# Optimization experiments

Measured on AMD Instinct MI355X. Metric: run time of the kernel, lower is better.

## Reference

```python
import jax, jax.numpy as jnp
import numpy as np

B, L, D, N = 4, 8192, 128, 32


def setup_inputs() -> dict:
    key = jax.random.key(0)
    ks = jax.random.split(key, 12)
    s = 0.05  # small init scale for stability of exp/cumsum
    return {
        "x": jax.random.normal(ks[0], (B, L, D), jnp.float32),
        "h_t_minus_1": jax.random.normal(ks[1], (B, L, D), jnp.float32),
        "A_log": jax.random.normal(ks[2], (D, N), jnp.float32),
        "D_param": jnp.ones((D,), jnp.float32),
        "W_x": jax.random.normal(ks[3], (D, 2 * N + D), jnp.float32) * s,
        "W_dt": jax.random.normal(ks[4], (D, D), jnp.float32) * s,
        "b_dt": jnp.zeros((D,), jnp.float32),
        "conv_w": jax.random.normal(ks[5], (3, D, D), jnp.float32) * s,  # (width, in, out)
        "conv_b": jnp.zeros((D,), jnp.float32),
        "W_f": jax.random.normal(ks[6], (D, D), jnp.float32) * s,
        "b_f": jnp.zeros((D,), jnp.float32),
    }


def reference(x, h_t_minus_1, A_log, D_param, W_x, W_dt, b_dt, conv_w, conv_b, W_f, b_f):
    d, n = A_log.shape
    A = -jnp.exp(A_log)  # (d, n)
    x_dbl = x @ W_x  # (b, l, d + 2n)
    delta, Bm, Cm = jnp.split(x_dbl, [d, d + n], axis=-1)
    delta = jax.nn.softplus(delta @ W_dt + b_dt)  # (b, l, d)

    # selective scan
    dA = jnp.einsum('bld,dn->bldn', delta, A)
    dB_u = jnp.einsum('bld,bld,bln->bldn', delta, h_t_minus_1, Bm)
    dA_cumsum = jnp.exp(jnp.cumsum(dA, axis=1) - dA)  # exclusive cumsum
    h_t = jnp.einsum('bldn,bln->bld', dB_u * dA_cumsum, Cm)
    h_t = h_t + h_t * D_param

    ssm_output = jax.nn.relu(h_t @ W_f + b_f)
    # causal Conv1D, kernel=3: left-pad by 2
    conv = jax.lax.conv_general_dilated(
        ssm_output, conv_w, window_strides=(1,), padding=[(2, 0)],
        dimension_numbers=('NWC', 'WIO', 'NWC')) + conv_b
    causal_output = jax.nn.relu(conv)
    fused_output = ssm_output * causal_output
    return (fused_output, h_t)
```

## Files before the change

kernel.cpp:

```cpp
#include <hip/hip_runtime.h>
#include <math.h>

typedef unsigned short u16;
typedef __attribute__((ext_vector_type(8))) short short8v;
typedef __attribute__((ext_vector_type(4))) float f32x4;

constexpr int B_  = 4;
constexpr int L_  = 8192;
constexpr int D_  = 128;
constexpr int N_  = 32;
constexpr int BL  = B_ * L_;
constexpr int CH  = 16;
constexpr int NC  = L_ / CH;
constexpr int SCH = 32;
constexpr int SNC = L_ / SCH;

__device__ inline unsigned bfr(float x) {
    unsigned u = __float_as_uint(x);
    return (u + 0x7fffu + ((u >> 16) & 1u)) >> 16;
}
__device__ inline unsigned pkbf(float a, float b) { return bfr(a) | (bfr(b) << 16); }
__device__ inline float b2f(u16 h) { return __uint_as_float(((unsigned)h) << 16); }

__global__ __launch_bounds__(256) void prep(
    const float* __restrict__ Wx, const float* __restrict__ Wdt,
    const float* __restrict__ Wf, const float* __restrict__ Wconv,
    const float* __restrict__ A_log,
    u16* __restrict__ Wt0, u16* __restrict__ Wt2, u16* __restrict__ Wtc,
    float* __restrict__ negA)
{
    const int which = blockIdx.y;
    const int t = blockIdx.x * 256 + threadIdx.x;
    if (which == 0) {
        if (t >= 128 * 128) return;
        const int d = t >> 7, k = t & 127;
        float s = 0.f;
        for (int j = 0; j < 128; ++j)
            s = fmaf(Wx[(size_t)k * 192 + j], Wdt[(size_t)j * 128 + d], s);
        Wt0[d * 128 + k] = (u16)bfr(s);
    } else if (which == 1) {
        if (t >= 64 * 128) return;
        const int n = t >> 7, k = t & 127;
        Wt0[(128 + n) * 128 + k] = (u16)bfr(Wx[(size_t)k * 192 + 128 + n]);
    } else if (which == 2) {
        if (t >= 128 * 128) return;
        const int n = t >> 7, k = t & 127;
        Wt2[n * 128 + k] = (u16)bfr(Wf[(size_t)k * 128 + n]);
    } else if (which <= 5) {
        if (t >= 128 * 128) return;
        const int w = which - 3;
        const int n = t >> 7, k = t & 127;
        Wtc[((size_t)w * 128 + n) * 128 + k] = (u16)bfr(Wconv[((size_t)w * 128 + k) * 128 + n]);
    } else {
        if (t < D_ * N_) negA[t] = -expf(A_log[t]) * 1.4426950408889634f;
    }
}

__global__ __launch_bounds__(512) void gemm1(
    const float* __restrict__ x, const u16* __restrict__ Wt0,
    const float* __restrict__ b_dt,
    float* __restrict__ delta, float* __restrict__ bc, float* __restrict__ part)
{
    __shared__ __align__(16) u16 Alds[64 * 64];
    __shared__ __align__(16) u16 Blds[192 * 64];

    const int tid = threadIdx.x;
    const int r0 = blockIdx.x * 64;
    const int wid = tid >> 6, lane = tid & 63;
    const int wm = wid >> 1, wn = wid & 1;
    const int lr = lane & 15, kg = lane >> 4;

    f32x4 acc[6] = {};

    for (int kt = 0; kt < 128; kt += 64) {
        {
            const int row = tid >> 3, k8 = (tid & 7) * 8;
            const float* src = &x[(size_t)(r0 + row) * 128 + kt + k8];
            const float4 v0 = *reinterpret_cast<const float4*>(src);
            const float4 v1 = *reinterpret_cast<const float4*>(src + 4);
            uint4 p;
            p.x = pkbf(v0.x, v0.y); p.y = pkbf(v0.z, v0.w);
            p.z = pkbf(v1.x, v1.y); p.w = pkbf(v1.z, v1.w);
            *reinterpret_cast<uint4*>(&Alds[row * 64 + (k8 ^ ((row & 7) << 3))]) = p;
        }
        #pragma unroll
        for (int j = 0; j < 3; ++j) {
            const int g = tid + j * 512;
            const int n = g >> 3, k8 = (g & 7) * 8;
            const uint4 p = *reinterpret_cast<const uint4*>(&Wt0[(size_t)n * 128 + kt + k8]);
            *reinterpret_cast<uint4*>(&Blds[n * 64 + (k8 ^ ((n & 7) << 3))]) = p;
        }
        __syncthreads();
        #pragma unroll
        for (int ks = 0; ks < 2; ++ks) {
            const int k8 = ks * 32 + kg * 8;
            const int row = wm * 16 + lr;
            const short8v af = *reinterpret_cast<const short8v*>(
                &Alds[row * 64 + (k8 ^ ((row & 7) << 3))]);
            #pragma unroll
            for (int nf = 0; nf < 6; ++nf) {
                const int col = wn * 96 + nf * 16 + lr;
                const short8v bf = *reinterpret_cast<const short8v*>(
                    &Blds[col * 64 + (k8 ^ ((col & 7) << 3))]);
                acc[nf] = __builtin_amdgcn_mfma_f32_16x16x32_bf16(af, bf, acc[nf], 0, 0, 0);
            }
        }
        __syncthreads();
    }

    const int nDelta = wn ? 2 : 6;
    float colsum[6];
    #pragma unroll
    for (int nf = 0; nf < 6; ++nf) {
        if (nf < nDelta) {
            const int col = wn * 96 + nf * 16 + lr;
            const float bb = b_dt[col];
            float s4 = 0.f;
            #pragma unroll
            for (int q = 0; q < 4; ++q) {
                float v = acc[nf][q] + bb;
                v = fmaxf(v, 0.f) + log1pf(expf(-fabsf(v)));
                const int row = r0 + wm * 16 + kg * 4 + q;
                delta[(size_t)row * 128 + col] = v;
                s4 += v;
            }
            colsum[nf] = s4;
        }
    }
    if (wn) {
        #pragma unroll
        for (int h = 0; h < 2; ++h)
            #pragma unroll
            for (int q = 0; q < 4; ++q) {
                const int row = r0 + wm * 16 + kg * 4 + q;
                bc[(size_t)row * 32 + h * 16 + lr] = acc[2 + h][q] * acc[4 + h][q];
            }
    }
    const int b = r0 / L_;
    const int c = (r0 % L_) / CH + wm;
    #pragma unroll
    for (int nf = 0; nf < 6; ++nf) {
        if (nf < nDelta) {
            float s = colsum[nf];
            s += __shfl_xor(s, 16, 64);
            s += __shfl_xor(s, 32, 64);
            if (kg == 0) {
                const int col = wn * 96 + nf * 16 + lr;
                part[((size_t)b * NC + c) * 128 + col] = s;
            }
        }
    }
}

__global__ __launch_bounds__(512) void scan_prefix(float* __restrict__ part)
{
    const int b = blockIdx.x, d = blockIdx.y;
    const int c = threadIdx.x, w = c >> 6, lane = c & 63;
    const size_t idx = ((size_t)b * NC + c) * 128 + d;
    const float v = part[idx];
    float s = v;
    #pragma unroll
    for (int off = 1; off < 64; off <<= 1) {
        const float t = __shfl_up(s, off, 64);
        if (lane >= off) s += t;
    }
    __shared__ float wsum[8];
    if (lane == 63) wsum[w] = s;
    __syncthreads();
    float add = 0.f;
    #pragma unroll
    for (int i = 0; i < 8; ++i)
        if (i < w) add += wsum[i];
    part[idx] = s + add - v;
}

__global__ __launch_bounds__(512) void scan_main(
    const float* __restrict__ delta, const float* __restrict__ hprev,
    const float* __restrict__ bc, const float* __restrict__ negA,
    const float* __restrict__ Dp, const float* __restrict__ part,
    const u16* __restrict__ Wt2, const float* __restrict__ b_f,
    float* __restrict__ h_out, u16* __restrict__ ssm)
{
    __shared__ float delta_s[SCH][128];
    __shared__ float bc_s[SCH][32];
    __shared__ __align__(16) u16 h_s[SCH * 128];

    const int cb = blockIdx.x, b = blockIdx.y;
    const int tid = threadIdx.x;
    const size_t rowbase = (size_t)b * L_ + (size_t)cb * SCH;

    #pragma unroll
    for (int j = 0; j < 2; ++j) {
        const int gg = tid + j * 512;
        const int row = gg >> 5, c4 = (gg & 31) * 4;
        *reinterpret_cast<float4*>(&delta_s[row][c4]) =
            *reinterpret_cast<const float4*>(&delta[(rowbase + row) * 128 + c4]);
    }
    if (tid < 256) {
        const int row = tid >> 3, c4 = (tid & 7) * 4;
        *reinterpret_cast<float4*>(&bc_s[row][c4]) =
            *reinterpret_cast<const float4*>(&bc[(rowbase + row) * 32 + c4]);
    }

    const int d = tid & 127, r0 = tid >> 7;
    float a[N_];
    #pragma unroll
    for (int n4 = 0; n4 < 8; ++n4) {
        const float4 v = *reinterpret_cast<const float4*>(&negA[d * N_ + n4 * 4]);
        a[n4 * 4 + 0] = v.x; a[n4 * 4 + 1] = v.y;
        a[n4 * 4 + 2] = v.z; a[n4 * 4 + 3] = v.w;
    }
    const float dp1 = 1.f + Dp[d];
    float hv[8];
    #pragma unroll
    for (int r = 0; r < 8; ++r)
        hv[r] = hprev[(rowbase + r * 4 + r0) * 128 + d];
    const float sbase = part[((size_t)b * NC + cb * 2) * 128 + d];
    __syncthreads();

    float sv[8];
    {
        float s = sbase;
        #pragma unroll
        for (int i = 0; i < 32; ++i) {
            if ((i & 3) == r0) sv[i >> 2] = s;
            s += delta_s[i][d];
        }
    }
    #pragma unroll
    for (int r = 0; r < 8; ++r) {
        const int i = r * 4 + r0;
        const float dv = delta_s[i][d];
        const float sr = sv[r];
        float p0 = 0.f, p1 = 0.f, p2 = 0.f, p3 = 0.f;
        #pragma unroll
        for (int n = 0; n < N_; n += 4) {
            const float4 b4 = *reinterpret_cast<const float4*>(&bc_s[i][n]);
            p0 = fmaf(b4.x, exp2f(sr * a[n + 0]), p0);
            p1 = fmaf(b4.y, exp2f(sr * a[n + 1]), p1);
            p2 = fmaf(b4.z, exp2f(sr * a[n + 2]), p2);
            p3 = fmaf(b4.w, exp2f(sr * a[n + 3]), p3);
        }
        const float h = dv * hv[r] * ((p0 + p1) + (p2 + p3)) * dp1;
        h_out[(rowbase + i) * 128 + d] = h;
        h_s[i * 128 + (((d >> 3) ^ (i & 7)) << 3) + (d & 7)] = (u16)bfr(h);
    }
    __syncthreads();

    const int wid = tid >> 6, lane = tid & 63;
    const int lr = lane & 15, kg = lane >> 4;
    const int col = wid * 16 + lr;
    f32x4 acc[2] = {};
    #pragma unroll
    for (int ks = 0; ks < 4; ++ks) {
        const int k8 = ks * 32 + kg * 8;
        const short8v bfg = *reinterpret_cast<const short8v*>(&Wt2[(size_t)col * 128 + k8]);
        #pragma unroll
        for (int m = 0; m < 2; ++m) {
            const int row = m * 16 + lr;
            const short8v afg = *reinterpret_cast<const short8v*>(
                &h_s[row * 128 + (k8 ^ ((row & 7) << 3))]);
            acc[m] = __builtin_amdgcn_mfma_f32_16x16x32_bf16(afg, bfg, acc[m], 0, 0, 0);
        }
    }
    const float bb = b_f[col];
    #pragma unroll
    for (int m = 0; m < 2; ++m)
        #pragma unroll
        for (int q = 0; q < 4; ++q) {
            const int row = m * 16 + kg * 4 + q;
            const float v = fmaxf(acc[m][q] + bb, 0.f);
            ssm[(rowbase + row) * 128 + col] = (u16)bfr(v);
        }
}

__global__ __launch_bounds__(512) void conv_fuse(
    const u16* __restrict__ ssm, const u16* __restrict__ Wtc,
    const float* __restrict__ cbias, float* __restrict__ fused)
{
    __shared__ __align__(16) u16 Alds[130 * 128];

    const int tid = threadIdx.x;
    const int bb = blockIdx.y;
    const int r0 = blockIdx.x * 128;
    const u16* sb = ssm + (size_t)bb * L_ * 128;

    #pragma unroll
    for (int j = 0; j < 5; ++j) {
        const int g = tid + j * 512;
        if (g < 130 * 16) {
            const int i = g >> 4, k8 = (g & 15) * 8;
            const int gr = r0 - 2 + i;
            uint4 p = make_uint4(0, 0, 0, 0);
            if (gr >= 0)
                p = *reinterpret_cast<const uint4*>(&sb[(size_t)gr * 128 + k8]);
            *reinterpret_cast<uint4*>(&Alds[i * 128 + (k8 ^ ((i & 7) << 3))]) = p;
        }
    }
    __syncthreads();

    const int wid = tid >> 6, lane = tid & 63;
    const int wm = wid >> 1, wn = wid & 1;
    const int lr = lane & 15, kg = lane >> 4;

    f32x4 acc[2][4] = {};
    #pragma unroll
    for (int ks = 0; ks < 4; ++ks) {
        const int k8 = ks * 32 + kg * 8;
        short8v af[2][3];
        #pragma unroll
        for (int m = 0; m < 2; ++m)
            #pragma unroll
            for (int w = 0; w < 3; ++w) {
                const int ri = wm * 32 + m * 16 + lr + w;
                af[m][w] = *reinterpret_cast<const short8v*>(
                    &Alds[ri * 128 + (k8 ^ ((ri & 7) << 3))]);
            }
        #pragma unroll
        for (int nf = 0; nf < 4; ++nf) {
            const int col = wn * 64 + nf * 16 + lr;
            #pragma unroll
            for (int w = 0; w < 3; ++w) {
                const short8v bfg = *reinterpret_cast<const short8v*>(
                    &Wtc[((size_t)w * 128 + col) * 128 + k8]);
                acc[0][nf] = __builtin_amdgcn_mfma_f32_16x16x32_bf16(af[0][w], bfg, acc[0][nf], 0, 0, 0);
                acc[1][nf] = __builtin_amdgcn_mfma_f32_16x16x32_bf16(af[1][w], bfg, acc[1][nf], 0, 0, 0);
            }
        }
    }

    #pragma unroll
    for (int nf = 0; nf < 4; ++nf) {
        const int col = wn * 64 + nf * 16 + lr;
        const float bb2 = cbias[col];
        #pragma unroll
        for (int m = 0; m < 2; ++m)
            #pragma unroll
            for (int q = 0; q < 4; ++q) {
                const int row = wm * 32 + m * 16 + kg * 4 + q;
                const int ri = row + 2;
                const u16 sh = Alds[ri * 128 + ((((col >> 3) ^ (ri & 7)) << 3)) + (col & 7)];
                const float cv = fmaxf(acc[m][nf][q] + bb2, 0.f);
                fused[((size_t)bb * L_ + r0 + row) * 128 + col] = b2f(sh) * cv;
            }
    }
}

extern "C" void kernel_launch(void* const* d_in, const int* in_sizes, int n_in,
                              void* d_out, int out_size, void* d_ws, size_t ws_size,
                              hipStream_t stream)
{
    const float* x      = (const float*)d_in[0];
    const float* hprev  = (const float*)d_in[1];
    const float* A_log  = (const float*)d_in[2];
    const float* Dp     = (const float*)d_in[3];
    const float* W_x    = (const float*)d_in[4];
    const float* W_dt   = (const float*)d_in[5];
    const float* b_dt   = (const float*)d_in[6];
    const float* conv_w = (const float*)d_in[7];
    const float* conv_b = (const float*)d_in[8];
    const float* W_f    = (const float*)d_in[9];
    const float* b_f    = (const float*)d_in[10];

    float* out   = (float*)d_out;
    float* h_out = out + (size_t)BL * D_;

    char* ws = (char*)d_ws;
    float* delta = (float*)ws;                  ws += (size_t)BL * 128 * 4;
    float* bcb   = (float*)ws;                  ws += (size_t)BL * 32 * 4;
    float* part  = (float*)ws;                  ws += (size_t)B_ * NC * 128 * 4;
    float* negA  = (float*)ws;                  ws += (size_t)D_ * N_ * 4;
    u16*   Wt0   = (u16*)ws;                    ws += (size_t)192 * 128 * 2;
    u16*   Wt2   = (u16*)ws;                    ws += (size_t)128 * 128 * 2;
    u16*   Wtc   = (u16*)ws;                    ws += (size_t)3 * 128 * 128 * 2;
    u16*   ssm   = (u16*)ws;

    prep<<<dim3(64, 7), dim3(256), 0, stream>>>(
        W_x, W_dt, W_f, conv_w, A_log, Wt0, Wt2, Wtc, negA);
    gemm1<<<dim3(BL / 64), dim3(512), 0, stream>>>(
        x, Wt0, b_dt, delta, bcb, part);
    scan_prefix<<<dim3(B_, D_), dim3(512), 0, stream>>>(part);
    scan_main<<<dim3(SNC, B_), dim3(512), 0, stream>>>(
        delta, hprev, bcb, negA, Dp, part, Wt2, b_f, h_out, ssm);
    conv_fuse<<<dim3(L_ / 128, B_), dim3(512), 0, stream>>>(
        ssm, Wtc, conv_b, out);
}
```

Baseline: 175.5 us.

## Reorder scan loops to cut registers, halve conv tile, coalesce prep reads

```diff
diff --git a/kernel.cpp b/kernel.cpp
--- a/kernel.cpp
+++ b/kernel.cpp
@@ -33,7 +33,7 @@
     const int t = blockIdx.x * 256 + threadIdx.x;
     if (which == 0) {
         if (t >= 128 * 128) return;
-        const int d = t >> 7, k = t & 127;
+        const int k = t >> 7, d = t & 127;
         float s = 0.f;
         for (int j = 0; j < 128; ++j)
             s = fmaf(Wx[(size_t)k * 192 + j], Wdt[(size_t)j * 128 + d], s);
@@ -203,13 +203,6 @@
     }
 
     const int d = tid & 127, r0 = tid >> 7;
-    float a[N_];
-    #pragma unroll
-    for (int n4 = 0; n4 < 8; ++n4) {
-        const float4 v = *reinterpret_cast<const float4*>(&negA[d * N_ + n4 * 4]);
-        a[n4 * 4 + 0] = v.x; a[n4 * 4 + 1] = v.y;
-        a[n4 * 4 + 2] = v.z; a[n4 * 4 + 3] = v.w;
-    }
     const float dp1 = 1.f + Dp[d];
     float hv[8];
     #pragma unroll
@@ -227,21 +220,30 @@
             s += delta_s[i][d];
         }
     }
+
+    float p[8] = {};
+    #pragma unroll 2
+    for (int n4 = 0; n4 < 8; ++n4) {
+        const float4 a4 = *reinterpret_cast<const float4*>(&negA[d * N_ + n4 * 4]);
+        #pragma unroll
+        for (int r = 0; r < 8; ++r) {
+            const int i = r * 4 + r0;
+            const float4 b4 = *reinterpret_cast<const float4*>(&bc_s[i][n4 * 4]);
+            const float sr = sv[r];
+            const float e0 = exp2f(sr * a4.x);
+            const float e1 = exp2f(sr * a4.y);
+            const float e2 = exp2f(sr * a4.z);
+            const float e3 = exp2f(sr * a4.w);
+            float t0 = fmaf(b4.x, e0, b4.y * e1);
+            float t1 = fmaf(b4.z, e2, b4.w * e3);
+            p[r] += t0 + t1;
+        }
+    }
+
     #pragma unroll
     for (int r = 0; r < 8; ++r) {
         const int i = r * 4 + r0;
-        const float dv = delta_s[i][d];
-        const float sr = sv[r];
-        float p0 = 0.f, p1 = 0.f, p2 = 0.f, p3 = 0.f;
-        #pragma unroll
-        for (int n = 0; n < N_; n += 4) {
-            const float4 b4 = *reinterpret_cast<const float4*>(&bc_s[i][n]);
-            p0 = fmaf(b4.x, exp2f(sr * a[n + 0]), p0);
-            p1 = fmaf(b4.y, exp2f(sr * a[n + 1]), p1);
-            p2 = fmaf(b4.z, exp2f(sr * a[n + 2]), p2);
-            p3 = fmaf(b4.w, exp2f(sr * a[n + 3]), p3);
-        }
-        const float h = dv * hv[r] * ((p0 + p1) + (p2 + p3)) * dp1;
+        const float h = delta_s[i][d] * hv[r] * p[r] * dp1;
         h_out[(rowbase + i) * 128 + d] = h;
         h_s[i * 128 + (((d >> 3) ^ (i & 7)) << 3) + (d & 7)] = (u16)bfr(h);
     }
@@ -278,17 +280,17 @@
     const u16* __restrict__ ssm, const u16* __restrict__ Wtc,
     const float* __restrict__ cbias, float* __restrict__ fused)
 {
-    __shared__ __align__(16) u16 Alds[130 * 128];
+    __shared__ __align__(16) u16 Alds[66 * 128];
 
     const int tid = threadIdx.x;
     const int bb = blockIdx.y;
-    const int r0 = blockIdx.x * 128;
+    const int r0 = blockIdx.x * 64;
     const u16* sb = ssm + (size_t)bb * L_ * 128;
 
     #pragma unroll
-    for (int j = 0; j < 5; ++j) {
+    for (int j = 0; j < 3; ++j) {
         const int g = tid + j * 512;
-        if (g < 130 * 16) {
+        if (g < 66 * 16) {
             const int i = g >> 4, k8 = (g & 15) * 8;
             const int gr = r0 - 2 + i;
             uint4 p = make_uint4(0, 0, 0, 0);
@@ -300,10 +302,10 @@
     __syncthreads();
 
     const int wid = tid >> 6, lane = tid & 63;
-    const int wm = wid >> 1, wn = wid & 1;
+    const int wm = wid >> 2, wn = wid & 3;
     const int lr = lane & 15, kg = lane >> 4;
 
-    f32x4 acc[2][4] = {};
+    f32x4 acc[2][2] = {};
     #pragma unroll
     for (int ks = 0; ks < 4; ++ks) {
         const int k8 = ks * 32 + kg * 8;
@@ -317,8 +319,8 @@
                     &Alds[ri * 128 + (k8 ^ ((ri & 7) << 3))]);
             }
         #pragma unroll
-        for (int nf = 0; nf < 4; ++nf) {
-            const int col = wn * 64 + nf * 16 + lr;
+        for (int nf = 0; nf < 2; ++nf) {
+            const int col = wn * 32 + nf * 16 + lr;
             #pragma unroll
             for (int w = 0; w < 3; ++w) {
                 const short8v bfg = *reinterpret_cast<const short8v*>(
@@ -330,8 +332,8 @@
     }
 
     #pragma unroll
-    for (int nf = 0; nf < 4; ++nf) {
-        const int col = wn * 64 + nf * 16 + lr;
+    for (int nf = 0; nf < 2; ++nf) {
+        const int col = wn * 32 + nf * 16 + lr;
         const float bb2 = cbias[col];
         #pragma unroll
         for (int m = 0; m < 2; ++m)
@@ -382,6 +384,6 @@
     scan_prefix<<<dim3(B_, D_), dim3(512), 0, stream>>>(part);
     scan_main<<<dim3(SNC, B_), dim3(512), 0, stream>>>(
         delta, hprev, bcb, negA, Dp, part, Wt2, b_f, h_out, ssm);
-    conv_fuse<<<dim3(L_ / 128, B_), dim3(512), 0, stream>>>(
+    conv_fuse<<<dim3(L_ / 64, B_), dim3(512), 0, stream>>>(
         ssm, Wtc, conv_b, out);
 }
```

Result: slower. 179.0 us (+2.0%).

## Restructure pipeline: local prefix in gemm1, row-parallel scan, fuse W_f GEMM into conv

Applied to the files above, without the earlier changes.

```diff
diff --git a/kernel.cpp b/kernel.cpp
--- a/kernel.cpp
+++ b/kernel.cpp
@@ -12,8 +12,6 @@
 constexpr int BL  = B_ * L_;
 constexpr int CH  = 16;
 constexpr int NC  = L_ / CH;
-constexpr int SCH = 32;
-constexpr int SNC = L_ / SCH;
 
 __device__ inline unsigned bfr(float x) {
     unsigned u = __float_as_uint(x);
@@ -22,33 +20,47 @@
 __device__ inline unsigned pkbf(float a, float b) { return bfr(a) | (bfr(b) << 16); }
 __device__ inline float b2f(u16 h) { return __uint_as_float(((unsigned)h) << 16); }
 
-__global__ __launch_bounds__(256) void prep(
+__global__ __launch_bounds__(512) void prep_weff(
     const float* __restrict__ Wx, const float* __restrict__ Wdt,
-    const float* __restrict__ Wf, const float* __restrict__ Wconv,
-    const float* __restrict__ A_log,
+    u16* __restrict__ Wt0)
+{
+    __shared__ float wd[128 * 128];
+    const int tid = threadIdx.x;
+    #pragma unroll
+    for (int j = 0; j < 8; ++j) {
+        const int g = tid + j * 512;
+        *reinterpret_cast<float4*>(&wd[g * 4]) =
+            *reinterpret_cast<const float4*>(&Wdt[(size_t)g * 4]);
+    }
+    __syncthreads();
+    const int k = blockIdx.x * 4 + (tid >> 7);
+    const int d = tid & 127;
+    float s = 0.f;
+    #pragma unroll 8
+    for (int j = 0; j < 128; ++j)
+        s = fmaf(Wx[(size_t)k * 192 + j], wd[j * 128 + d], s);
+    Wt0[d * 128 + k] = (u16)bfr(s);
+}
+
+__global__ __launch_bounds__(256) void prep_rest(
+    const float* __restrict__ Wx, const float* __restrict__ Wf,
+    const float* __restrict__ Wconv, const float* __restrict__ A_log,
     u16* __restrict__ Wt0, u16* __restrict__ Wt2, u16* __restrict__ Wtc,
     float* __restrict__ negA)
 {
     const int which = blockIdx.y;
     const int t = blockIdx.x * 256 + threadIdx.x;
     if (which == 0) {
-        if (t >= 128 * 128) return;
-        const int d = t >> 7, k = t & 127;
-        float s = 0.f;
-        for (int j = 0; j < 128; ++j)
-            s = fmaf(Wx[(size_t)k * 192 + j], Wdt[(size_t)j * 128 + d], s);
-        Wt0[d * 128 + k] = (u16)bfr(s);
-    } else if (which == 1) {
         if (t >= 64 * 128) return;
         const int n = t >> 7, k = t & 127;
         Wt0[(128 + n) * 128 + k] = (u16)bfr(Wx[(size_t)k * 192 + 128 + n]);
-    } else if (which == 2) {
+    } else if (which == 1) {
         if (t >= 128 * 128) return;
         const int n = t >> 7, k = t & 127;
         Wt2[n * 128 + k] = (u16)bfr(Wf[(size_t)k * 128 + n]);
-    } else if (which <= 5) {
+    } else if (which <= 4) {
         if (t >= 128 * 128) return;
-        const int w = which - 3;
+        const int w = which - 2;
         const int n = t >> 7, k = t & 127;
         Wtc[((size_t)w * 128 + n) * 128 + k] = (u16)bfr(Wconv[((size_t)w * 128 + k) * 128 + n]);
     } else {
@@ -56,100 +68,96 @@
     }
 }
 
-__global__ __launch_bounds__(512) void gemm1(
+__global__ __launch_bounds__(256) void gemm1(
     const float* __restrict__ x, const u16* __restrict__ Wt0,
     const float* __restrict__ b_dt,
-    float* __restrict__ delta, float* __restrict__ bc, float* __restrict__ part)
-{
-    __shared__ __align__(16) u16 Alds[64 * 64];
-    __shared__ __align__(16) u16 Blds[192 * 64];
+    float* __restrict__ delta, float* __restrict__ Sloc,
+    float* __restrict__ bc, float* __restrict__ part)
+{
+    __shared__ __align__(16) u16 Blds[192 * 128];
 
     const int tid = threadIdx.x;
     const int r0 = blockIdx.x * 64;
-    const int wid = tid >> 6, lane = tid & 63;
-    const int wm = wid >> 1, wn = wid & 1;
+
+    #pragma unroll
+    for (int j = 0; j < 12; ++j) {
+        const int g = tid + j * 256;
+        const int n = g >> 4, k8 = (g & 15) * 8;
+        const uint4 p = *reinterpret_cast<const uint4*>(&Wt0[(size_t)n * 128 + k8]);
+        *reinterpret_cast<uint4*>(&Blds[n * 128 + (k8 ^ ((n & 7) << 3))]) = p;
+    }
+
+    const int w = tid >> 6, lane = tid & 63;
     const int lr = lane & 15, kg = lane >> 4;
-
-    f32x4 acc[6] = {};
-
-    for (int kt = 0; kt < 128; kt += 64) {
-        {
-            const int row = tid >> 3, k8 = (tid & 7) * 8;
-            const float* src = &x[(size_t)(r0 + row) * 128 + kt + k8];
-            const float4 v0 = *reinterpret_cast<const float4*>(src);
-            const float4 v1 = *reinterpret_cast<const float4*>(src + 4);
-            uint4 p;
-            p.x = pkbf(v0.x, v0.y); p.y = pkbf(v0.z, v0.w);
-            p.z = pkbf(v1.x, v1.y); p.w = pkbf(v1.z, v1.w);
-            *reinterpret_cast<uint4*>(&Alds[row * 64 + (k8 ^ ((row & 7) << 3))]) = p;
-        }
-        #pragma unroll
-        for (int j = 0; j < 3; ++j) {
-            const int g = tid + j * 512;
-            const int n = g >> 3, k8 = (g & 7) * 8;
-            const uint4 p = *reinterpret_cast<const uint4*>(&Wt0[(size_t)n * 128 + kt + k8]);
-            *reinterpret_cast<uint4*>(&Blds[n * 64 + (k8 ^ ((n & 7) << 3))]) = p;
-        }
-        __syncthreads();
-        #pragma unroll
-        for (int ks = 0; ks < 2; ++ks) {
-            const int k8 = ks * 32 + kg * 8;
-            const int row = wm * 16 + lr;
-            const short8v af = *reinterpret_cast<const short8v*>(
-                &Alds[row * 64 + (k8 ^ ((row & 7) << 3))]);
-            #pragma unroll
-            for (int nf = 0; nf < 6; ++nf) {
-                const int col = wn * 96 + nf * 16 + lr;
-                const short8v bf = *reinterpret_cast<const short8v*>(
-                    &Blds[col * 64 + (k8 ^ ((col & 7) << 3))]);
-                acc[nf] = __builtin_amdgcn_mfma_f32_16x16x32_bf16(af, bf, acc[nf], 0, 0, 0);
-            }
-        }
-        __syncthreads();
-    }
-
-    const int nDelta = wn ? 2 : 6;
-    float colsum[6];
-    #pragma unroll
-    for (int nf = 0; nf < 6; ++nf) {
-        if (nf < nDelta) {
-            const int col = wn * 96 + nf * 16 + lr;
-            const float bb = b_dt[col];
-            float s4 = 0.f;
-            #pragma unroll
-            for (int q = 0; q < 4; ++q) {
-                float v = acc[nf][q] + bb;
-                v = fmaxf(v, 0.f) + log1pf(expf(-fabsf(v)));
-                const int row = r0 + wm * 16 + kg * 4 + q;
-                delta[(size_t)row * 128 + col] = v;
-                s4 += v;
-            }
-            colsum[nf] = s4;
-        }
-    }
-    if (wn) {
-        #pragma unroll
-        for (int h = 0; h < 2; ++h)
-            #pragma unroll
-            for (int q = 0; q < 4; ++q) {
-                const int row = r0 + wm * 16 + kg * 4 + q;
-                bc[(size_t)row * 32 + h * 16 + lr] = acc[2 + h][q] * acc[4 + h][q];
-            }
-    }
-    const int b = r0 / L_;
-    const int c = (r0 % L_) / CH + wm;
-    #pragma unroll
-    for (int nf = 0; nf < 6; ++nf) {
-        if (nf < nDelta) {
-            float s = colsum[nf];
-            s += __shfl_xor(s, 16, 64);
-            s += __shfl_xor(s, 32, 64);
-            if (kg == 0) {
-                const int col = wn * 96 + nf * 16 + lr;
-                part[((size_t)b * NC + c) * 128 + col] = s;
-            }
-        }
-    }
+    const int arow = r0 + w * 16 + lr;
+
+    float4 av[4][2];
+    #pragma unroll
+    for (int ks = 0; ks < 4; ++ks) {
+        const float* src = &x[(size_t)arow * 128 + ks * 32 + kg * 8];
+        av[ks][0] = *reinterpret_cast<const float4*>(src);
+        av[ks][1] = *reinterpret_cast<const float4*>(src + 4);
+    }
+    __syncthreads();
+
+    f32x4 acc[12] = {};
+    #pragma unroll
+    for (int ks = 0; ks < 4; ++ks) {
+        uint4 ap;
+        ap.x = pkbf(av[ks][0].x, av[ks][0].y);
+        ap.y = pkbf(av[ks][0].z, av[ks][0].w);
+        ap.z = pkbf(av[ks][1].x, av[ks][1].y);
+        ap.w = pkbf(av[ks][1].z, av[ks][1].w);
+        const short8v af = *reinterpret_cast<const short8v*>(&ap);
+        const int kb = ks * 32 + kg * 8;
+        #pragma unroll
+        for (int nf = 0; nf < 12; ++nf) {
+            const int n = nf * 16 + lr;
+            const short8v bf = *reinterpret_cast<const short8v*>(
+                &Blds[n * 128 + (kb ^ ((n & 7) << 3))]);
+            acc[nf] = __builtin_amdgcn_mfma_f32_16x16x32_bf16(af, bf, acc[nf], 0, 0, 0);
+        }
+    }
+
+    const int orow = r0 + w * 16;
+    const size_t chunkb = (size_t)(orow / CH) * 128;
+    #pragma unroll
+    for (int nf = 0; nf < 8; ++nf) {
+        const int col = nf * 16 + lr;
+        const float bb = b_dt[col];
+        float v[4];
+        #pragma unroll
+        for (int q = 0; q < 4; ++q) {
+            const float t = acc[nf][q] + bb;
+            v[q] = fmaxf(t, 0.f) + log1pf(expf(-fabsf(t)));
+        }
+        const float e1 = v[0], e2 = e1 + v[1], e3 = e2 + v[2];
+        const float g4 = e3 + v[3];
+        const float g0 = __shfl(g4, lr, 64);
+        const float g1 = __shfl(g4, lr + 16, 64);
+        const float g2 = __shfl(g4, lr + 32, 64);
+        const float g3 = __shfl(g4, lr + 48, 64);
+        float base = 0.f;
+        if (kg > 0) base += g0;
+        if (kg > 1) base += g1;
+        if (kg > 2) base += g2;
+        const size_t rb = (size_t)(orow + kg * 4) * 128 + col;
+        delta[rb + 0 * 128] = v[0];
+        delta[rb + 1 * 128] = v[1];
+        delta[rb + 2 * 128] = v[2];
+        delta[rb + 3 * 128] = v[3];
+        Sloc[rb + 0 * 128] = base;
+        Sloc[rb + 1 * 128] = base + e1;
+        Sloc[rb + 2 * 128] = base + e2;
+        Sloc[rb + 3 * 128] = base + e3;
+        if (kg == 0) part[chunkb + col] = g0 + g1 + g2 + g3;
+    }
+    #pragma unroll
+    for (int h = 0; h < 2; ++h)
+        #pragma unroll
+        for (int q = 0; q < 4; ++q)
+            bc[(size_t)(orow + kg * 4 + q) * 32 + h * 16 + lr] =
+                acc[8 + h][q] * acc[10 + h][q];
 }
 
 __global__ __launch_bounds__(512) void scan_prefix(float* __restrict__ part)
@@ -174,35 +182,15 @@
     part[idx] = s + add - v;
 }
 
-__global__ __launch_bounds__(512) void scan_main(
-    const float* __restrict__ delta, const float* __restrict__ hprev,
-    const float* __restrict__ bc, const float* __restrict__ negA,
-    const float* __restrict__ Dp, const float* __restrict__ part,
-    const u16* __restrict__ Wt2, const float* __restrict__ b_f,
-    float* __restrict__ h_out, u16* __restrict__ ssm)
-{
-    __shared__ float delta_s[SCH][128];
-    __shared__ float bc_s[SCH][32];
-    __shared__ __align__(16) u16 h_s[SCH * 128];
-
-    const int cb = blockIdx.x, b = blockIdx.y;
+__global__ __launch_bounds__(512) void scan_h(
+    const float* __restrict__ delta, const float* __restrict__ Sloc,
+    const float* __restrict__ hprev, const float* __restrict__ bc,
+    const float* __restrict__ negA, const float* __restrict__ Dp,
+    const float* __restrict__ part,
+    float* __restrict__ h_out, u16* __restrict__ hb)
+{
     const int tid = threadIdx.x;
-    const size_t rowbase = (size_t)b * L_ + (size_t)cb * SCH;
-
-    #pragma unroll
-    for (int j = 0; j < 2; ++j) {
-        const int gg = tid + j * 512;
-        const int row = gg >> 5, c4 = (gg & 31) * 4;
-        *reinterpret_cast<float4*>(&delta_s[row][c4]) =
-            *reinterpret_cast<const float4*>(&delta[(rowbase + row) * 128 + c4]);
-    }
-    if (tid < 256) {
-        const int row = tid >> 3, c4 = (tid & 7) * 4;
-        *reinterpret_cast<float4*>(&bc_s[row][c4]) =
-            *reinterpret_cast<const float4*>(&bc[(rowbase + row) * 32 + c4]);
-    }
-
-    const int d = tid & 127, r0 = tid >> 7;
+    const int d = tid & 127;
     float a[N_];
     #pragma unroll
     for (int n4 = 0; n4 < 8; ++n4) {
@@ -211,138 +199,123 @@
         a[n4 * 4 + 2] = v.z; a[n4 * 4 + 3] = v.w;
     }
     const float dp1 = 1.f + Dp[d];
-    float hv[8];
-    #pragma unroll
-    for (int r = 0; r < 8; ++r)
-        hv[r] = hprev[(rowbase + r * 4 + r0) * 128 + d];
-    const float sbase = part[((size_t)b * NC + cb * 2) * 128 + d];
-    __syncthreads();
-
-    float sv[8];
-    {
-        float s = sbase;
-        #pragma unroll
-        for (int i = 0; i < 32; ++i) {
-            if ((i & 3) == r0) sv[i >> 2] = s;
-            s += delta_s[i][d];
-        }
-    }
-    #pragma unroll
-    for (int r = 0; r < 8; ++r) {
-        const int i = r * 4 + r0;
-        const float dv = delta_s[i][d];
-        const float sr = sv[r];
+
+    #pragma unroll
+    for (int it = 0; it < 4; ++it) {
+        const size_t row = ((size_t)blockIdx.x + (size_t)it * 2048) * 4 + (tid >> 7);
+        const size_t rb = row * 128 + d;
+        const float dv = delta[rb];
+        const float sl = Sloc[rb];
+        const float hv = hprev[rb];
+        const float S = part[(row >> 4) * 128 + d] + sl;
         float p0 = 0.f, p1 = 0.f, p2 = 0.f, p3 = 0.f;
         #pragma unroll
-        for (int n = 0; n < N_; n += 4) {
-            const float4 b4 = *reinterpret_cast<const float4*>(&bc_s[i][n]);
-            p0 = fmaf(b4.x, exp2f(sr * a[n + 0]), p0);
-            p1 = fmaf(b4.y, exp2f(sr * a[n + 1]), p1);
-            p2 = fmaf(b4.z, exp2f(sr * a[n + 2]), p2);
-            p3 = fmaf(b4.w, exp2f(sr * a[n + 3]), p3);
-        }
-        const float h = dv * hv[r] * ((p0 + p1) + (p2 + p3)) * dp1;
-        h_out[(rowbase + i) * 128 + d] = h;
-        h_s[i * 128 + (((d >> 3) ^ (i & 7)) << 3) + (d & 7)] = (u16)bfr(h);
-    }
-    __syncthreads();
-
-    const int wid = tid >> 6, lane = tid & 63;
-    const int lr = lane & 15, kg = lane >> 4;
-    const int col = wid * 16 + lr;
-    f32x4 acc[2] = {};
-    #pragma unroll
-    for (int ks = 0; ks < 4; ++ks) {
-        const int k8 = ks * 32 + kg * 8;
-        const short8v bfg = *reinterpret_cast<const short8v*>(&Wt2[(size_t)col * 128 + k8]);
-        #pragma unroll
-        for (int m = 0; m < 2; ++m) {
-            const int row = m * 16 + lr;
-            const short8v afg = *reinterpret_cast<const short8v*>(
-                &h_s[row * 128 + (k8 ^ ((row & 7) << 3))]);
-            acc[m] = __builtin_amdgcn_mfma_f32_16x16x32_bf16(afg, bfg, acc[m], 0, 0, 0);
-        }
-    }
-    const float bb = b_f[col];
-    #pragma unroll
-    for (int m = 0; m < 2; ++m)
-        #pragma unroll
-        for (int q = 0; q < 4; ++q) {
-            const int row = m * 16 + kg * 4 + q;
-            const float v = fmaxf(acc[m][q] + bb, 0.f);
-            ssm[(rowbase + row) * 128 + col] = (u16)bfr(v);
-        }
-}
-
-__global__ __launch_bounds__(512) void conv_fuse(
-    const u16* __restrict__ ssm, const u16* __restrict__ Wtc,
+        for (int n4 = 0; n4 < 8; ++n4) {
+            const float4 b4 = *reinterpret_cast<const float4*>(&bc[row * 32 + n4 * 4]);
+            p0 = fmaf(b4.x, exp2f(S * a[n4 * 4 + 0]), p0);
+            p1 = fmaf(b4.y, exp2f(S * a[n4 * 4 + 1]), p1);
+            p2 = fmaf(b4.z, exp2f(S * a[n4 * 4 + 2]), p2);
+            p3 = fmaf(b4.w, exp2f(S * a[n4 * 4 + 3]), p3);
+        }
+        const float h = dv * hv * ((p0 + p1) + (p2 + p3)) * dp1;
+        h_out[rb] = h;
+        hb[rb] = (u16)bfr(h);
+    }
+}
+
+__global__ __launch_bounds__(256) void conv_fuse2(
+    const u16* __restrict__ hb, const u16* __restrict__ Wt2,
+    const float* __restrict__ b_f, const u16* __restrict__ Wtc,
     const float* __restrict__ cbias, float* __restrict__ fused)
 {
-    __shared__ __align__(16) u16 Alds[130 * 128];
+    __shared__ __align__(16) u16 hb_s[80 * 128];
+    __shared__ __align__(16) u16 ssm_s[80 * 128];
 
     const int tid = threadIdx.x;
     const int bb = blockIdx.y;
-    const int r0 = blockIdx.x * 128;
-    const u16* sb = ssm + (size_t)bb * L_ * 128;
+    const int r0 = blockIdx.x * 64;
+    const u16* hbB = hb + (size_t)bb * L_ * 128;
 
     #pragma unroll
     for (int j = 0; j < 5; ++j) {
-        const int g = tid + j * 512;
-        if (g < 130 * 16) {
-            const int i = g >> 4, k8 = (g & 15) * 8;
-            const int gr = r0 - 2 + i;
-            uint4 p = make_uint4(0, 0, 0, 0);
-            if (gr >= 0)
-                p = *reinterpret_cast<const uint4*>(&sb[(size_t)gr * 128 + k8]);
-            *reinterpret_cast<uint4*>(&Alds[i * 128 + (k8 ^ ((i & 7) << 3))]) = p;
-        }
-    }
-    __syncthreads();
-
-    const int wid = tid >> 6, lane = tid & 63;
-    const int wm = wid >> 1, wn = wid & 1;
+        const int g = tid + j * 256;
+        const int s = g >> 4, k8 = (g & 15) * 8;
+        const int grow = r0 - 2 + s;
+        uint4 p = make_uint4(0, 0, 0, 0);
+        if (grow >= 0 && grow < L_)
+            p = *reinterpret_cast<const uint4*>(&hbB[(size_t)grow * 128 + k8]);
+        *reinterpret_cast<uint4*>(&hb_s[s * 128 + (k8 ^ ((s & 7) << 3))]) = p;
+    }
+    __syncthreads();
+
+    const int w = tid >> 6, lane = tid & 63;
     const int lr = lane & 15, kg = lane >> 4;
 
-    f32x4 acc[2][4] = {};
-    #pragma unroll
-    for (int ks = 0; ks < 4; ++ks) {
-        const int k8 = ks * 32 + kg * 8;
-        short8v af[2][3];
-        #pragma unroll
-        for (int m = 0; m < 2; ++m)
+    for (int sm = w; sm < 5; sm += 4) {
+        f32x4 acc[8] = {};
+        #pragma unroll
+        for (int ks = 0; ks < 4; ++ks) {
+            const int kb = ks * 32 + kg * 8;
+            const int sr = sm * 16 + lr;
+            const short8v af = *reinterpret_cast<const short8v*>(
+                &hb_s[sr * 128 + (kb ^ ((sr & 7) << 3))]);
             #pragma unroll
-            for (int w = 0; w < 3; ++w) {
-                const int ri = wm * 32 + m * 16 + lr + w;
-                af[m][w] = *reinterpret_cast<const short8v*>(
-                    &Alds[ri * 128 + (k8 ^ ((ri & 7) << 3))]);
+            for (int nf = 0; nf < 8; ++nf) {
+                const int col = nf * 16 + lr;
+                const short8v bf = *reinterpret_cast<const short8v*>(
+                    &Wt2[(size_t)col * 128 + kb]);
+                acc[nf] = __builtin_amdgcn_mfma_f32_16x16x32_bf16(af, bf, acc[nf], 0, 0, 0);
             }
-        #pragma unroll
-        for (int nf = 0; nf < 4; ++nf) {
-            const int col = wn * 64 + nf * 16 + lr;
-            #pragma unroll
-            for (int w = 0; w < 3; ++w) {
-                const short8v bfg = *reinterpret_cast<const short8v*>(
-                    &Wtc[((size_t)w * 128 + col) * 128 + k8]);
-                acc[0][nf] = __builtin_amdgcn_mfma_f32_16x16x32_bf16(af[0][w], bfg, acc[0][nf], 0, 0, 0);
-                acc[1][nf] = __builtin_amdgcn_mfma_f32_16x16x32_bf16(af[1][w], bfg, acc[1][nf], 0, 0, 0);
-            }
-        }
-    }
-
-    #pragma unroll
-    for (int nf = 0; nf < 4; ++nf) {
-        const int col = wn * 64 + nf * 16 + lr;
-        const float bb2 = cbias[col];
-        #pragma unroll
-        for (int m = 0; m < 2; ++m)
+        }
+        #pragma unroll
+        for (int nf = 0; nf < 8; ++nf) {
+            const int col = nf * 16 + lr;
+            const float bbv = b_f[col];
             #pragma unroll
             for (int q = 0; q < 4; ++q) {
-                const int row = wm * 32 + m * 16 + kg * 4 + q;
-                const int ri = row + 2;
-                const u16 sh = Alds[ri * 128 + ((((col >> 3) ^ (ri & 7)) << 3)) + (col & 7)];
-                const float cv = fmaxf(acc[m][nf][q] + bb2, 0.f);
-                fused[((size_t)bb * L_ + r0 + row) * 128 + col] = b2f(sh) * cv;
+                const int s2 = sm * 16 + kg * 4 + q;
+                float vv = fmaxf(acc[nf][q] + bbv, 0.f);
+                if (r0 - 2 + s2 < 0) vv = 0.f;
+                ssm_s[s2 * 128 + (col ^ ((s2 & 7) << 3))] = (u16)bfr(vv);
             }
+        }
+    }
+    __syncthreads();
+
+    f32x4 acc[8] = {};
+    #pragma unroll
+    for (int ks = 0; ks < 4; ++ks) {
+        const int kb = ks * 32 + kg * 8;
+        short8v af[3];
+        #pragma unroll
+        for (int t = 0; t < 3; ++t) {
+            const int sr = w * 16 + lr + t;
+            af[t] = *reinterpret_cast<const short8v*>(
+                &ssm_s[sr * 128 + (kb ^ ((sr & 7) << 3))]);
+        }
+        #pragma unroll
+        for (int nf = 0; nf < 8; ++nf) {
+            const int col = nf * 16 + lr;
+            #pragma unroll
+            for (int t = 0; t < 3; ++t) {
+                const short8v bf = *reinterpret_cast<const short8v*>(
+                    &Wtc[((size_t)t * 128 + col) * 128 + kb]);
+                acc[nf] = __builtin_amdgcn_mfma_f32_16x16x32_bf16(af[t], bf, acc[nf], 0, 0, 0);
+            }
+        }
+    }
+    #pragma unroll
+    for (int nf = 0; nf < 8; ++nf) {
+        const int col = nf * 16 + lr;
+        const float cbv = cbias[col];
+        #pragma unroll
+        for (int q = 0; q < 4; ++q) {
+            const int ro = w * 16 + kg * 4 + q;
+            const int s2 = ro + 2;
+            const u16 sv = ssm_s[s2 * 128 + (col ^ ((s2 & 7) << 3))];
+            const float cv = fmaxf(acc[nf][q] + cbv, 0.f);
+            fused[((size_t)bb * L_ + r0 + ro) * 128 + col] = b2f(sv) * cv;
+        }
     }
 }
 
@@ -367,21 +340,23 @@
 
     char* ws = (char*)d_ws;
     float* delta = (float*)ws;                  ws += (size_t)BL * 128 * 4;
+    float* sloc  = (float*)ws;                  ws += (size_t)BL * 128 * 4;
     float* bcb   = (float*)ws;                  ws += (size_t)BL * 32 * 4;
     float* part  = (float*)ws;                  ws += (size_t)B_ * NC * 128 * 4;
     float* negA  = (float*)ws;                  ws += (size_t)D_ * N_ * 4;
     u16*   Wt0   = (u16*)ws;                    ws += (size_t)192 * 128 * 2;
     u16*   Wt2   = (u16*)ws;                    ws += (size_t)128 * 128 * 2;
     u16*   Wtc   = (u16*)ws;                    ws += (size_t)3 * 128 * 128 * 2;
-    u16*   ssm   = (u16*)ws;
-
-    prep<<<dim3(64, 7), dim3(256), 0, stream>>>(
-        W_x, W_dt, W_f, conv_w, A_log, Wt0, Wt2, Wtc, negA);
-    gemm1<<<dim3(BL / 64), dim3(512), 0, stream>>>(
-        x, Wt0, b_dt, delta, bcb, part);
+    u16*   hb    = (u16*)ws;
+
+    prep_weff<<<dim3(32), dim3(512), 0, stream>>>(W_x, W_dt, Wt0);
+    prep_rest<<<dim3(64, 6), dim3(256), 0, stream>>>(
+        W_x, W_f, conv_w, A_log, Wt0, Wt2, Wtc, negA);
+    gemm1<<<dim3(BL / 64), dim3(256), 0, stream>>>(
+        x, Wt0, b_dt, delta, sloc, bcb, part);
     scan_prefix<<<dim3(B_, D_), dim3(512), 0, stream>>>(part);
-    scan_main<<<dim3(SNC, B_), dim3(512), 0, stream>>>(
-        delta, hprev, bcb, negA, Dp, part, Wt2, b_f, h_out, ssm);
-    conv_fuse<<<dim3(L_ / 128, B_), dim3(512), 0, stream>>>(
-        ssm, Wtc, conv_b, out);
-}
+    scan_h<<<dim3(2048), dim3(512), 0, stream>>>(
+        delta, sloc, hprev, bcb, negA, Dp, part, h_out, hb);
+    conv_fuse2<<<dim3(L_ / 64, B_), dim3(256), 0, stream>>>(
+        hb, Wt2, b_f, Wtc, conv_b, out);
+}
```

New measurement: 198.5 us. 13.1% more time.
